# Kernel optimization log

Hardware: AMD Instinct MI355X
Metric: run time of the kernel (lower is better)

Reference implementation:

```python
import jax, jax.numpy as jnp
import numpy as np

H, BS, NB, R, K = 2048, 128, 44, 64, 8   # hidden, block_size, num_blocks, basis_rank, top_k
B, S = 4, 2048
I = NB * BS                               # intermediate size = 5632


def setup_inputs() -> dict:
    key = jax.random.key(0)
    ks = jax.random.split(key, 10)
    N = B * S
    return {
        "hidden_states": jax.random.normal(ks[0], (B, S, H), jnp.float32),
        "active_idx": jax.random.randint(ks[1], (N, K), 0, NB, jnp.int32),
        "active_score": jax.random.uniform(ks[2], (N, K), dtype=jnp.float32),
        "gate_w": jax.random.normal(ks[3], (I, H), jnp.float32) * 0.02,
        "up_w": jax.random.normal(ks[4], (I, H), jnp.float32) * 0.02,
        "down_w": jax.random.normal(ks[5], (H, I), jnp.float32) * 0.02,
        "enc_w": jax.random.normal(ks[6], (R, H), jnp.float32) * 0.02,
        "enc_b": jnp.zeros((R,), jnp.float32),
        "decoder": jax.random.normal(ks[7], (NB, R, BS), jnp.float32) * 0.02,
        "basis_bias": jnp.zeros((NB, BS), jnp.float32),
        "comp_bias": jnp.zeros((H,), jnp.float32),
        "scale": jnp.array(1.0, jnp.float32),
    }


def reference(hidden_states, active_idx, active_score, gate_w, up_w, down_w,
              enc_w, enc_b, decoder, basis_bias, comp_bias, scale):
    Bb, Ss, Hh = hidden_states.shape
    N = Bb * Ss
    x = hidden_states.reshape(N, Hh)                          # [N, H]

    # routing weights: softmax over selected block scores (all idx valid here),
    # scattered into a dense per-token per-block weight map (duplicates accumulate)
    w = jax.nn.softmax(active_score, axis=-1)                 # [N, K]
    block_w = jnp.zeros((N, NB), x.dtype).at[
        jnp.arange(N)[:, None], active_idx].add(w)            # [N, NB]

    # gated SiLU MLP intermediate over all blocks (dense equivalent of the
    # per-token block gather-compute)
    act = jax.nn.silu(x @ gate_w.T) * (x @ up_w.T)            # [N, I]

    # low-rank basis compensation: latent -> per-block block_size channels
    latent = jax.nn.silu(x @ enc_w.T + enc_b)                 # [N, R]
    comp = jnp.einsum('nr,brc->nbc', latent, decoder) + basis_bias  # [N, NB, BS]

    act_b = act.reshape(N, NB, BS) + scale * comp             # [N, NB, BS]
    weighted = (act_b * block_w[:, :, None]).reshape(N, I)    # mask+weight inactive blocks to 0

    out = weighted @ down_w.T + comp_bias                     # scatter back via down proj
    return out.reshape(Bb, Ss, Hh)
```

## Files before the change

kernel.cpp:

```cpp
#include <hip/hip_runtime.h>

#define H_  2048
#define BS_ 128
#define NB_ 44
#define R_  64
#define K_  8
#define N_  8192
#define I_  5632
#define MT  64
#define TILES 32
#define GRID_AB (8 * 6 * TILES)
#define MT2 128
#define TILES_GU 16
#define GRID_GU (8 * 6 * TILES_GU)

typedef __bf16 bf16x8 __attribute__((ext_vector_type(8)));
typedef float  f32x4  __attribute__((ext_vector_type(4)));

__device__ __forceinline__ unsigned short f2bf(float f) {
  unsigned int u = __float_as_uint(f);
  u = (u + 0x7FFFu + ((u >> 16) & 1u)) >> 16;
  return (unsigned short)u;
}
__device__ __forceinline__ float bf2f(unsigned short s) {
  return __uint_as_float(((unsigned int)s) << 16);
}
__device__ __forceinline__ bf16x8 ld8(const unsigned short* p) {
  uint4 v = *reinterpret_cast<const uint4*>(p);
  return __builtin_bit_cast(bf16x8, v);
}
__device__ __forceinline__ bf16x8 lds8(const char* p) {
  uint4 v = *reinterpret_cast<const uint4*>(p);
  return __builtin_bit_cast(bf16x8, v);
}
__device__ __forceinline__ void gl16(const void* g, void* l) {
  __builtin_amdgcn_global_load_lds(
      (const __attribute__((address_space(1))) char*)g,
      (__attribute__((address_space(3))) char*)l, 16, 0, 0);
}
#define WAIT_VM(n) do { asm volatile("s_waitcnt vmcnt(" #n ")" ::: "memory"); \
                        __builtin_amdgcn_sched_barrier(0); } while (0)
#define WAIT_LGKM0 do { asm volatile("s_waitcnt lgkmcnt(0)" ::: "memory"); \
                        __builtin_amdgcn_sched_barrier(0); } while (0)
#define SBAR __builtin_amdgcn_s_barrier()

__global__ void cvt_xgu(const float* __restrict__ x, const float* __restrict__ gw,
                        const float* __restrict__ uw, const float* __restrict__ ew,
                        const float* __restrict__ dw,
                        unsigned short* __restrict__ xb,
                        unsigned short* __restrict__ gwb,
                        unsigned short* __restrict__ uwb,
                        unsigned short* __restrict__ ewb,
                        unsigned short* __restrict__ dwb,
                        int do_down) {
  const int NX4 = N_ * H_ / 4;
  const int NG4 = I_ * H_ / 4;
  const int NE4 = R_ * H_ / 4;
  const int ND4 = H_ * I_ / 4;
  int total = NX4 + 2 * NG4 + NE4 + (do_down ? ND4 : 0);
  int stride = gridDim.x * blockDim.x;
  for (int i = blockIdx.x * blockDim.x + threadIdx.x; i < total; i += stride) {
    if (i < NX4 + 2 * NG4 + NE4) {
      const float4* s; ushort4* d; int j;
      if (i < NX4)                  { s = (const float4*)x;  d = (ushort4*)xb;  j = i; }
      else if (i < NX4 + NG4)       { s = (const float4*)gw; d = (ushort4*)gwb; j = i - NX4; }
      else if (i < NX4 + 2 * NG4)   { s = (const float4*)uw; d = (ushort4*)uwb; j = i - NX4 - NG4; }
      else                          { s = (const float4*)ew; d = (ushort4*)ewb; j = i - NX4 - 2 * NG4; }
      float4 v = s[j];
      ushort4 o; o.x = f2bf(v.x); o.y = f2bf(v.y); o.z = f2bf(v.z); o.w = f2bf(v.w);
      d[j] = o;
    } else {
      int j = i - (NX4 + 2 * NG4 + NE4);
      float4 v = ((const float4*)dw)[j];
      int flat = j * 4;
      int h = flat / I_;
      int rem = flat - h * I_;
      int b = rem >> 7, k = rem & 127;
      ushort4 o; o.x = f2bf(v.x); o.y = f2bf(v.y); o.z = f2bf(v.z); o.w = f2bf(v.w);
      *(ushort4*)(dwb + ((size_t)b * H_ + h) * BS_ + k) = o;
    }
  }
}

__global__ void cvt_down(const float* __restrict__ dw, unsigned short* __restrict__ dwb) {
  int total = H_ * I_ / 4;
  int stride = gridDim.x * blockDim.x;
  for (int i = blockIdx.x * blockDim.x + threadIdx.x; i < total; i += stride) {
    float4 v = ((const float4*)dw)[i];
    int flat = i * 4;
    int h = flat / I_;
    int rem = flat - h * I_;
    int b = rem >> 7, k = rem & 127;
    ushort4 o; o.x = f2bf(v.x); o.y = f2bf(v.y); o.z = f2bf(v.z); o.w = f2bf(v.w);
    *(ushort4*)(dwb + ((size_t)b * H_ + h) * BS_ + k) = o;
  }
}

__global__ void cvt_dec(const float* __restrict__ dec, unsigned short* __restrict__ decb) {
  int i = blockIdx.x * 256 + threadIdx.x;
  if (i >= NB_ * BS_ * R_) return;
  int b = i >> 13;
  int rem = i & 8191;
  int c = rem >> 6, r = rem & 63;
  decb[i] = f2bf(dec[(b << 13) + r * BS_ + c]);
}

__global__ void zero_counts(int* __restrict__ counts) {
  if (threadIdx.x < NB_) counts[threadIdx.x] = 0;
}

__global__ void prep_kernel(const float* __restrict__ score,
                            const int* __restrict__ aidx,
                            float* __restrict__ w_buf,
                            int* __restrict__ counts) {
  __shared__ int hist[NB_];
  int tid = threadIdx.x;
  if (tid < NB_) hist[tid] = 0;
  __syncthreads();
  int n = blockIdx.x * 256 + tid;
  float s[K_];
  float m = -1e30f;
#pragma unroll
  for (int k = 0; k < K_; k++) { s[k] = score[n * K_ + k]; m = fmaxf(m, s[k]); }
  float sum = 0.f;
#pragma unroll
  for (int k = 0; k < K_; k++) { s[k] = __expf(s[k] - m); sum += s[k]; }
  float inv = 1.f / sum;
#pragma unroll
  for (int k = 0; k < K_; k++) {
    w_buf[n * K_ + k] = s[k] * inv;
    atomicAdd(&hist[aidx[n * K_ + k]], 1);
  }
  __syncthreads();
  if (tid < NB_) atomicAdd(&counts[tid], hist[tid]);
}

__global__ void scan_kernel(const int* __restrict__ counts,
                            int* __restrict__ offsets,
                            int* __restrict__ cursors) {
  if (threadIdx.x == 0) {
    int acc = 0;
    for (int b = 0; b < NB_; b++) { offsets[b] = acc; cursors[b] = acc; acc += counts[b]; }
    offsets[NB_] = acc;
  }
}

__global__ void fill_kernel(const int* __restrict__ aidx,
                            const float* __restrict__ w_buf,
                            int* __restrict__ cursors,
                            int* __restrict__ tok_list,
                            float* __restrict__ wt_list,
                            int* __restrict__ inv) {
  int n = blockIdx.x * 256 + threadIdx.x;
#pragma unroll
  for (int k = 0; k < K_; k++) {
    int b = aidx[n * K_ + k];
    int pos = atomicAdd(&cursors[b], 1);
    tok_list[pos] = n;
    wt_list[pos] = w_buf[n * K_ + k];
    inv[n * K_ + k] = pos;
  }
}

__global__ __launch_bounds__(256) void latent_mfma(
    const unsigned short* __restrict__ xb,
    const unsigned short* __restrict__ ewb,
    const float* __restrict__ enc_b,
    unsigned short* __restrict__ lat) {
  __shared__ __align__(16) char smem[16384];
  int tid = threadIdx.x;
  int wv = tid >> 6, lane = tid & 63;
  int lo = lane & 15, hi = lane >> 4;
  int n0 = blockIdx.x * 64;

  int rowA = tid >> 2;
  int jA = (tid & 3) ^ ((rowA >> 1) & 3);
  const unsigned short* srcA = xb + (size_t)(n0 + rowA) * H_ + jA * 8;
  const unsigned short* srcB = ewb + (size_t)rowA * H_ + jA * 8;

  gl16(srcA, smem + wv * 1024);
  gl16(srcB, smem + 8192 + wv * 1024);

  f32x4 acc[4] = {};
  int cur = 0;
  for (int ks = 0; ks < H_; ks += 32) {
    if (ks + 32 < H_) {
      gl16(srcA + ks + 32, smem + (cur ^ 1) * 4096 + wv * 1024);
      gl16(srcB + ks + 32, smem + 8192 + (cur ^ 1) * 4096 + wv * 1024);
      WAIT_VM(2);
    } else {
      WAIT_VM(0);
    }
    SBAR;
    int rB = wv * 16 + lo;
    bf16x8 Bf = lds8(smem + 8192 + cur * 4096 + (rB * 4 + (hi ^ ((rB >> 1) & 3))) * 16);
#pragma unroll
    for (int m = 0; m < 4; m++) {
      int row = m * 16 + lo;
      bf16x8 Af = lds8(smem + cur * 4096 + (row * 4 + (hi ^ ((row >> 1) & 3))) * 16);
      acc[m] = __builtin_amdgcn_mfma_f32_16x16x32_bf16(Af, Bf, acc[m], 0, 0, 0);
    }
    WAIT_LGKM0;
    SBAR;
    cur ^= 1;
  }

  int r = wv * 16 + lo;
  float eb = enc_b[r];
#pragma unroll
  for (int m = 0; m < 4; m++) {
#pragma unroll
    for (int rg = 0; rg < 4; rg++) {
      int tok = n0 + m * 16 + hi * 4 + rg;
      float v = acc[m][rg] + eb;
      lat[(size_t)tok * R_ + r] = f2bf(v / (1.f + __expf(-v)));
    }
  }
}

__device__ __forceinline__ bool decode_bt(int p, int& b, int& tile) {
  b = (p & 7) + 8 * ((p >> 3) / TILES);
  tile = (p >> 3) % TILES;
  return b < NB_;
}
__device__ __forceinline__ bool decode_bt_gu(int p, int& b, int& tile) {
  b = (p & 7) + 8 * ((p >> 3) / TILES_GU);
  tile = (p >> 3) % TILES_GU;
  return b < NB_;
}

__global__ __launch_bounds__(512, 4) void gateup_kernel(
    const unsigned short* __restrict__ xb,
    const unsigned short* __restrict__ gwb,
    const unsigned short* __restrict__ uwb,
    const unsigned short* __restrict__ latb,
    const unsigned short* __restrict__ decb_all,
    const float* __restrict__ bbias,
    const float* __restrict__ scale_p,
    const int* __restrict__ counts,
    const int* __restrict__ offsets,
    const int* __restrict__ tok_list,
    const float* __restrict__ wt_list,
    unsigned short* __restrict__ actw) {
  int b, tile;
  if (!decode_bt_gu(blockIdx.x, b, tile)) return;
  int cnt = counts[b];
  int base = tile * MT2;
  if (base >= cnt) return;
  int off = offsets[b];

  __shared__ __align__(16) char smem[49152];

  int tid = threadIdx.x;
  int wv = tid >> 6, lane = tid & 63;
  int lo = lane & 15, hi = lane >> 4;
  int wr = wv >> 2, wc = wv & 3;

  int rowA = tid >> 2;
  int jA = (tid & 3) ^ ((rowA >> 1) & 3);
  int tokA = tok_list[off + min(base + rowA, cnt - 1)];
  const unsigned short* srcA = xb + (size_t)tokA * H_ + jA * 8;

  const unsigned short* gb = gwb + (size_t)b * BS_ * H_;
  const unsigned short* ub = uwb + (size_t)b * BS_ * H_;
  int cS = tid >> 2;
  int jS = (tid & 3) ^ ((cS >> 1) & 3);
  const unsigned short* srcG = gb + (size_t)cS * H_ + jS * 8;
  const unsigned short* srcU = ub + (size_t)cS * H_ + jS * 8;

  f32x4 accG[4][2] = {};
  f32x4 accU[4][2] = {};

  gl16(srcA, smem + wv * 1024);
  gl16(srcG, smem + 16384 + wv * 1024);
  gl16(srcU, smem + 32768 + wv * 1024);

  for (int it = 0; it < 64; ++it) {
    int ks = it * 32;
    if (it < 63) {
      int nb_ = (it + 1) & 1;
      gl16(srcA + ks + 32, smem + nb_ * 8192 + wv * 1024);
      gl16(srcG + ks + 32, smem + 16384 + nb_ * 8192 + wv * 1024);
      gl16(srcU + ks + 32, smem + 32768 + nb_ * 8192 + wv * 1024);
      WAIT_VM(3);
    } else {
      WAIT_VM(0);
    }
    SBAR;
    int cur = it & 1;
    bf16x8 Af[4];
#pragma unroll
    for (int m = 0; m < 4; m++) {
      int row = wr * 64 + m * 16 + lo;
      int off16 = row * 4 + (hi ^ ((row >> 1) & 3));
      Af[m] = lds8(smem + cur * 8192 + off16 * 16);
    }
    bf16x8 Gf[2], Uf[2];
#pragma unroll
    for (int cf = 0; cf < 2; cf++) {
      int c = wc * 32 + cf * 16 + lo;
      int off16 = c * 4 + (hi ^ ((c >> 1) & 3));
      Gf[cf] = lds8(smem + 16384 + cur * 8192 + off16 * 16);
      Uf[cf] = lds8(smem + 32768 + cur * 8192 + off16 * 16);
    }
#pragma unroll
    for (int m = 0; m < 4; m++) {
#pragma unroll
      for (int cf = 0; cf < 2; cf++) {
        accG[m][cf] = __builtin_amdgcn_mfma_f32_16x16x32_bf16(Af[m], Gf[cf], accG[m][cf], 0, 0, 0);
        accU[m][cf] = __builtin_amdgcn_mfma_f32_16x16x32_bf16(Af[m], Uf[cf], accU[m][cf], 0, 0, 0);
      }
    }
    WAIT_LGKM0;
    SBAR;
  }

#pragma unroll
  for (int s = 0; s < 2; s++) {
    int o = s * 512 + tid;
    int r_ = o >> 3;
    int j = (o & 7) ^ (r_ & 7);
    int tokL = tok_list[off + min(base + r_, cnt - 1)];
    gl16(latb + (size_t)tokL * R_ + j * 8, smem + 32768 + s * 8192 + wv * 1024);
  }
  const unsigned short* decb = decb_all + (size_t)b * BS_ * R_;
#pragma unroll
  for (int s = 0; s < 2; s++) {
    int o = s * 512 + tid;
    int c = o >> 3;
    int j = (o & 7) ^ (c & 7);
    gl16(decb + (size_t)c * R_ + j * 8, smem + 16384 + s * 8192 + wv * 1024);
  }
  __syncthreads();

  f32x4 accC[4][2] = {};
#pragma unroll
  for (int kk = 0; kk < 2; kk++) {
    bf16x8 L[4];
#pragma unroll
    for (int m = 0; m < 4; m++) {
      int row = wr * 64 + m * 16 + lo;
      int off16 = row * 8 + ((kk * 4 + hi) ^ (row & 7));
      L[m] = lds8(smem + 32768 + off16 * 16);
    }
#pragma unroll
    for (int cf = 0; cf < 2; cf++) {
      int c = wc * 32 + cf * 16 + lo;
      int off16 = c * 8 + ((kk * 4 + hi) ^ (c & 7));
      bf16x8 D = lds8(smem + 16384 + off16 * 16);
#pragma unroll
      for (int m = 0; m < 4; m++)
        accC[m][cf] = __builtin_amdgcn_mfma_f32_16x16x32_bf16(L[m], D, accC[m][cf], 0, 0, 0);
    }
  }

  float scal = scale_p[0];
  int cc[2] = { wc * 32 + lo, wc * 32 + 16 + lo };
  float bbv[2] = { bbias[b * BS_ + cc[0]], bbias[b * BS_ + cc[1]] };
#pragma unroll
  for (int m = 0; m < 4; m++) {
#pragma unroll
    for (int r = 0; r < 4; r++) {
      int t = wr * 64 + m * 16 + hi * 4 + r;
      int g = base + t;
      if (g < cnt) {
        float wt = wt_list[off + g];
        unsigned short* dst = actw + (size_t)(off + g) * BS_;
#pragma unroll
        for (int cf = 0; cf < 2; cf++) {
          float gg = accG[m][cf][r];
          float uu = accU[m][cf][r];
          float act = (gg / (1.f + __expf(-gg))) * uu;
          dst[cc[cf]] = f2bf((act + scal * (accC[m][cf][r] + bbv[cf])) * wt);
        }
      }
    }
  }
}

__global__ __launch_bounds__(256) void down_kernel(
    const unsigned short* __restrict__ actw,
    const unsigned short* __restrict__ dwb,
    const int* __restrict__ counts,
    const int* __restrict__ offsets,
    unsigned short* __restrict__ partial,
    int hc0, int Hc) {
  int b, tile;
  if (!decode_bt(blockIdx.x, b, tile)) return;
  int cnt = counts[b];
  int base = tile * MT;
  if (base >= cnt) return;
  int off = offsets[b];

  __shared__ __align__(16) unsigned short a_lds[MT * BS_];
  __shared__ __align__(16) char b_lds[2][16384];
  int tid = threadIdx.x;
  int wv = tid >> 6, lane = tid & 63;
  int lo = lane & 15, hi = lane >> 4;

  for (int i = tid; i < MT * BS_ / 8; i += 256) {
    int t = i >> 4, cb = i & 15;
    int g = base + t;
    uint4 v = make_uint4(0, 0, 0, 0);
    if (g < cnt) v = *(const uint4*)(actw + (size_t)(off + g) * BS_ + cb * 8);
    *(uint4*)(&a_lds[t * BS_ + ((cb ^ (t & 7)) << 3)]) = v;
  }
  __syncthreads();

  bf16x8 Bf[4][4];
#pragma unroll
  for (int kst = 0; kst < 4; kst++)
#pragma unroll
    for (int sf = 0; sf < 4; sf++) {
      int t = sf * 16 + lo, cb = kst * 4 + hi;
      Bf[kst][sf] = ld8(&a_lds[t * BS_ + ((cb ^ (t & 7)) << 3)]);
    }

  const unsigned short* db = dwb + (size_t)b * H_ * BS_;
  int rs = tid >> 4;
  int jc = tid & 15;
  {
    const unsigned short* d0 = db + (size_t)hc0 * BS_;
#pragma unroll
    for (int s = 0; s < 4; s++) {
      int r = s * 16 + rs;
      int j = jc ^ (r & 15);
      gl16(d0 + (size_t)r * BS_ + j * 8, b_lds[0] + s * 4096 + wv * 1024);
    }
  }
  __syncthreads();

  int nit = Hc >> 6;
  int cur = 0;
  for (int it = 0; it < nit; it++) {
    if (it + 1 < nit) {
      const unsigned short* dn = db + (size_t)(hc0 + (it + 1) * 64) * BS_;
#pragma unroll
      for (int s = 0; s < 4; s++) {
        int r = s * 16 + rs;
        int j = jc ^ (r & 15);
        gl16(dn + (size_t)r * BS_ + j * 8, b_lds[cur ^ 1] + s * 4096 + wv * 1024);
      }
    }
    f32x4 acc[4] = {};
    int rl = wv * 16 + lo;
#pragma unroll
    for (int kst = 0; kst < 4; kst++) {
      int cb = kst * 4 + hi;
      bf16x8 Aw = lds8(b_lds[cur] + (rl * 16 + (cb ^ lo)) * 16);
#pragma unroll
      for (int sf = 0; sf < 4; sf++)
        acc[sf] = __builtin_amdgcn_mfma_f32_16x16x32_bf16(Aw, Bf[kst][sf], acc[sf], 0, 0, 0);
    }
    int hrel = it * 64 + wv * 16 + hi * 4;
#pragma unroll
    for (int sf = 0; sf < 4; sf++) {
      int g = base + sf * 16 + lo;
      if (g < cnt) {
        uint2 pk;
        pk.x = (unsigned int)f2bf(acc[sf][0]) | ((unsigned int)f2bf(acc[sf][1]) << 16);
        pk.y = (unsigned int)f2bf(acc[sf][2]) | ((unsigned int)f2bf(acc[sf][3]) << 16);
        *(uint2*)(partial + (size_t)(off + g) * Hc + hrel) = pk;
      }
    }
    __syncthreads();
    cur ^= 1;
  }
}

__global__ __launch_bounds__(256) void reduce_kernel(
    const unsigned short* __restrict__ partial,
    const int* __restrict__ inv,
    const float* __restrict__ cbias,
    float* __restrict__ out, int hc0, int Hc) {
  int wv = threadIdx.x >> 6, l = threadIdx.x & 63;
  int n = blockIdx.x * 4 + wv;
  int rows[K_];
#pragma unroll
  for (int k = 0; k < K_; k++) rows[k] = inv[n * K_ + k];
  for (int c0w = 0; c0w < Hc; c0w += 512) {
    int cw = c0w + l * 8;
    if (cw >= Hc) continue;
    float a[8] = {0.f, 0.f, 0.f, 0.f, 0.f, 0.f, 0.f, 0.f};
#pragma unroll
    for (int k = 0; k < K_; k++) {
      uint4 v = *(const uint4*)(partial + (size_t)rows[k] * Hc + cw);
      unsigned int w0 = v.x, w1 = v.y, w2 = v.z, w3 = v.w;
      a[0] += __uint_as_float(w0 << 16); a[1] += __uint_as_float(w0 & 0xFFFF0000u);
      a[2] += __uint_as_float(w1 << 16); a[3] += __uint_as_float(w1 & 0xFFFF0000u);
      a[4] += __uint_as_float(w2 << 16); a[5] += __uint_as_float(w2 & 0xFFFF0000u);
      a[6] += __uint_as_float(w3 << 16); a[7] += __uint_as_float(w3 & 0xFFFF0000u);
    }
    int h = hc0 + cw;
    float4 c0 = *(const float4*)(cbias + h);
    float4 c1 = *(const float4*)(cbias + h + 4);
    float4 o0 = make_float4(a[0] + c0.x, a[1] + c0.y, a[2] + c0.z, a[3] + c0.w);
    float4 o1 = make_float4(a[4] + c1.x, a[5] + c1.y, a[6] + c1.z, a[7] + c1.w);
    *(float4*)(out + (size_t)n * H_ + h) = o0;
    *(float4*)(out + (size_t)n * H_ + h + 4) = o1;
  }
}

extern "C" void kernel_launch(void* const* d_in, const int* in_sizes, int n_in,
                              void* d_out, int out_size, void* d_ws, size_t ws_size,
                              hipStream_t stream) {
  const float* x       = (const float*)d_in[0];
  const int*   aidx    = (const int*)d_in[1];
  const float* score   = (const float*)d_in[2];
  const float* gate_w  = (const float*)d_in[3];
  const float* up_w    = (const float*)d_in[4];
  const float* down_w  = (const float*)d_in[5];
  const float* enc_w   = (const float*)d_in[6];
  const float* enc_b   = (const float*)d_in[7];
  const float* decoder = (const float*)d_in[8];
  const float* bbias   = (const float*)d_in[9];
  const float* cbias   = (const float*)d_in[10];
  const float* scale   = (const float*)d_in[11];
  float* out = (float*)d_out;

  char* ws = (char*)d_ws;
  const size_t OFF_GWB  = 33554432ull;
  const size_t OFF_UWB  = 56623104ull;
  const size_t OFF_DEC  = 79691776ull;
  const size_t OFF_LATB = 80412672ull;
  const size_t OFF_ENCB = 81461248ull;
  const size_t OFF_WBUF = 81723392ull;
  const size_t OFF_TOK  = 81985536ull;
  const size_t OFF_WT   = 82247680ull;
  const size_t OFF_INV  = 82509824ull;
  const size_t OFF_CNT  = 82771968ull;
  const size_t OFF_ACTW = 82772992ull;
  const size_t BASE_END = 99550208ull;
  const size_t DWB_SZ   = 23068672ull;

  unsigned short* xb   = (unsigned short*)(ws);
  unsigned short* gwb  = (unsigned short*)(ws + OFF_GWB);
  unsigned short* uwb  = (unsigned short*)(ws + OFF_UWB);
  unsigned short* decb = (unsigned short*)(ws + OFF_DEC);
  unsigned short* latb = (unsigned short*)(ws + OFF_LATB);
  unsigned short* ewb  = (unsigned short*)(ws + OFF_ENCB);
  float* w_buf         = (float*)(ws + OFF_WBUF);
  int*   tok_list      = (int*)(ws + OFF_TOK);
  float* wt_list       = (float*)(ws + OFF_WT);
  int*   inv           = (int*)(ws + OFF_INV);
  int*   counts        = (int*)(ws + OFF_CNT);
  int*   offsets       = counts + 64;
  int*   cursors       = counts + 128;
  unsigned short* actw = (unsigned short*)(ws + OFF_ACTW);

  int Hc; unsigned short* dwb; unsigned short* partial; bool early_down;
  if      (ws_size >= BASE_END + DWB_SZ + 131072ull * 512) Hc = 512;
  else if (ws_size >= BASE_END + DWB_SZ + 131072ull * 256) Hc = 256;
  else Hc = 0;
  if (Hc) {
    early_down = true;
    dwb = (unsigned short*)(ws + BASE_END);
    partial = (unsigned short*)(ws + BASE_END + DWB_SZ);
  } else {
    early_down = false;
    Hc = 256;
    dwb = gwb;
    partial = (unsigned short*)ws;
  }
  int nch = H_ / Hc;

  cvt_xgu<<<2048, 256, 0, stream>>>(x, gate_w, up_w, enc_w, down_w,
                                    xb, gwb, uwb, ewb, dwb, early_down ? 1 : 0);
  cvt_dec<<<(NB_ * BS_ * R_ + 255) / 256, 256, 0, stream>>>(decoder, decb);
  zero_counts<<<1, 64, 0, stream>>>(counts);
  prep_kernel<<<N_ / 256, 256, 0, stream>>>(score, aidx, w_buf, counts);
  scan_kernel<<<1, 64, 0, stream>>>(counts, offsets, cursors);
  fill_kernel<<<N_ / 256, 256, 0, stream>>>(aidx, w_buf, cursors, tok_list, wt_list, inv);
  latent_mfma<<<N_ / 64, 256, 0, stream>>>(xb, ewb, enc_b, latb);
  gateup_kernel<<<GRID_GU, 512, 0, stream>>>(xb, gwb, uwb, latb, decb, bbias, scale,
                                             counts, offsets, tok_list, wt_list, actw);
  if (!early_down) cvt_down<<<2048, 256, 0, stream>>>(down_w, dwb);
  for (int c = 0; c < nch; c++) {
    down_kernel<<<GRID_AB, 256, 0, stream>>>(actw, dwb, counts, offsets, partial, c * Hc, Hc);
    reduce_kernel<<<N_ / 4, 256, 0, stream>>>(partial, inv, cbias, out, c * Hc, Hc);
  }
}
```

Baseline: 548.5 us.

## Fuse down projection into gate/up kernel when workspace allows full partials

When the workspace is large enough, the gate/up kernel keeps its weighted activation tile in LDS and runs the down projection over all hidden columns directly, streaming double-buffered down_w tiles and writing bf16 partials for one reduce pass. This removes the actw round trip through global memory, the separate down_kernel launches and the chunked down/reduce loop. LDS grows to 64KB per block, which may cut occupancy. Each block now does a serial 32-step loop over the hidden dimension, which lengthens its lifetime. The fallback path now always converts down_w early instead of aliasing it onto the gate buffer.

```diff
diff --git a/kernel.cpp b/kernel.cpp
--- a/kernel.cpp
+++ b/kernel.cpp
@@ -82,20 +82,6 @@
   }
 }
 
-__global__ void cvt_down(const float* __restrict__ dw, unsigned short* __restrict__ dwb) {
-  int total = H_ * I_ / 4;
-  int stride = gridDim.x * blockDim.x;
-  for (int i = blockIdx.x * blockDim.x + threadIdx.x; i < total; i += stride) {
-    float4 v = ((const float4*)dw)[i];
-    int flat = i * 4;
-    int h = flat / I_;
-    int rem = flat - h * I_;
-    int b = rem >> 7, k = rem & 127;
-    ushort4 o; o.x = f2bf(v.x); o.y = f2bf(v.y); o.z = f2bf(v.z); o.w = f2bf(v.w);
-    *(ushort4*)(dwb + ((size_t)b * H_ + h) * BS_ + k) = o;
-  }
-}
-
 __global__ void cvt_dec(const float* __restrict__ dec, unsigned short* __restrict__ decb) {
   int i = blockIdx.x * 256 + threadIdx.x;
   if (i >= NB_ * BS_ * R_) return;
@@ -235,13 +221,16 @@
     const unsigned short* __restrict__ uwb,
     const unsigned short* __restrict__ latb,
     const unsigned short* __restrict__ decb_all,
+    const unsigned short* __restrict__ dwb,
     const float* __restrict__ bbias,
     const float* __restrict__ scale_p,
     const int* __restrict__ counts,
     const int* __restrict__ offsets,
     const int* __restrict__ tok_list,
     const float* __restrict__ wt_list,
-    unsigned short* __restrict__ actw) {
+    unsigned short* __restrict__ actw,
+    unsigned short* __restrict__ partial,
+    int fused) {
   int b, tile;
   if (!decode_bt_gu(blockIdx.x, b, tile)) return;
   int cnt = counts[b];
@@ -249,7 +238,7 @@
   if (base >= cnt) return;
   int off = offsets[b];
 
-  __shared__ __align__(16) char smem[49152];
+  __shared__ __align__(16) char smem[65536];
 
   int tid = threadIdx.x;
   int wv = tid >> 6, lane = tid & 63;
@@ -321,7 +310,7 @@
     int r_ = o >> 3;
     int j = (o & 7) ^ (r_ & 7);
     int tokL = tok_list[off + min(base + r_, cnt - 1)];
-    gl16(latb + (size_t)tokL * R_ + j * 8, smem + 32768 + s * 8192 + wv * 1024);
+    gl16(latb + (size_t)tokL * R_ + j * 8, smem + 49152 + s * 8192 + wv * 1024);
   }
   const unsigned short* decb = decb_all + (size_t)b * BS_ * R_;
 #pragma unroll
@@ -329,7 +318,7 @@
     int o = s * 512 + tid;
     int c = o >> 3;
     int j = (o & 7) ^ (c & 7);
-    gl16(decb + (size_t)c * R_ + j * 8, smem + 16384 + s * 8192 + wv * 1024);
+    gl16(decb + (size_t)c * R_ + j * 8, smem + 32768 + s * 8192 + wv * 1024);
   }
   __syncthreads();
 
@@ -341,13 +330,13 @@
     for (int m = 0; m < 4; m++) {
       int row = wr * 64 + m * 16 + lo;
       int off16 = row * 8 + ((kk * 4 + hi) ^ (row & 7));
-      L[m] = lds8(smem + 32768 + off16 * 16);
+      L[m] = lds8(smem + 49152 + off16 * 16);
     }
 #pragma unroll
     for (int cf = 0; cf < 2; cf++) {
       int c = wc * 32 + cf * 16 + lo;
       int off16 = c * 8 + ((kk * 4 + hi) ^ (c & 7));
-      bf16x8 D = lds8(smem + 16384 + off16 * 16);
+      bf16x8 D = lds8(smem + 32768 + off16 * 16);
 #pragma unroll
       for (int m = 0; m < 4; m++)
         accC[m][cf] = __builtin_amdgcn_mfma_f32_16x16x32_bf16(L[m], D, accC[m][cf], 0, 0, 0);
@@ -357,24 +346,121 @@
   float scal = scale_p[0];
   int cc[2] = { wc * 32 + lo, wc * 32 + 16 + lo };
   float bbv[2] = { bbias[b * BS_ + cc[0]], bbias[b * BS_ + cc[1]] };
+
+  if (!fused) {
+#pragma unroll
+    for (int m = 0; m < 4; m++) {
+#pragma unroll
+      for (int r = 0; r < 4; r++) {
+        int t = wr * 64 + m * 16 + hi * 4 + r;
+        int g = base + t;
+        if (g < cnt) {
+          float wt = wt_list[off + g];
+          unsigned short* dst = actw + (size_t)(off + g) * BS_;
+#pragma unroll
+          for (int cf = 0; cf < 2; cf++) {
+            float gg = accG[m][cf][r];
+            float uu = accU[m][cf][r];
+            float act = (gg / (1.f + __expf(-gg))) * uu;
+            dst[cc[cf]] = f2bf((act + scal * (accC[m][cf][r] + bbv[cf])) * wt);
+          }
+        }
+      }
+    }
+    return;
+  }
+
+  unsigned short* act_lds = (unsigned short*)smem;
 #pragma unroll
   for (int m = 0; m < 4; m++) {
 #pragma unroll
     for (int r = 0; r < 4; r++) {
       int t = wr * 64 + m * 16 + hi * 4 + r;
       int g = base + t;
+      float wt = (g < cnt) ? wt_list[off + g] : 0.f;
+#pragma unroll
+      for (int cf = 0; cf < 2; cf++) {
+        int c = cc[cf];
+        float gg = accG[m][cf][r];
+        float uu = accU[m][cf][r];
+        float act = (gg / (1.f + __expf(-gg))) * uu;
+        float a = (act + scal * (accC[m][cf][r] + bbv[cf])) * wt;
+        int cb2 = c >> 3;
+        act_lds[t * BS_ + (((cb2 ^ (t & 7)) << 3) | (c & 7))] = f2bf(a);
+      }
+    }
+  }
+  __syncthreads();
+
+  int wh = wv >> 2, ws2 = wv & 3;
+  bf16x8 Bact[4][2];
+#pragma unroll
+  for (int kst = 0; kst < 4; kst++)
+#pragma unroll
+    for (int sf = 0; sf < 2; sf++) {
+      int t = ws2 * 32 + sf * 16 + lo;
+      int cb = kst * 4 + hi;
+      Bact[kst][sf] = lds8(smem + t * 256 + ((cb ^ (t & 7)) << 4));
+    }
+
+  const unsigned short* db = dwb + (size_t)b * H_ * BS_;
+#pragma unroll
+  for (int s = 0; s < 2; s++) {
+    int o = s * 512 + tid;
+    int row = o >> 4;
+    int j = (o & 15) ^ (row & 15);
+    gl16(db + (size_t)row * BS_ + j * 8, smem + 32768 + s * 8192 + wv * 1024);
+  }
+  for (int it = 0; it < 32; ++it) {
+    int hc = it * 64;
+    if (it < 31) {
+      int nb_ = (it + 1) & 1;
+#pragma unroll
+      for (int s = 0; s < 2; s++) {
+        int o = s * 512 + tid;
+        int row = o >> 4;
+        int j = (o & 15) ^ (row & 15);
+        gl16(db + (size_t)(hc + 64 + row) * BS_ + j * 8,
+             smem + 32768 + nb_ * 16384 + s * 8192 + wv * 1024);
+      }
+      WAIT_VM(10);
+    } else {
+      WAIT_VM(8);
+    }
+    SBAR;
+    const char* bbuf = smem + 32768 + (it & 1) * 16384;
+    f32x4 acc2[2][2] = {};
+#pragma unroll
+    for (int kst = 0; kst < 4; kst++) {
+      int cb = kst * 4 + hi;
+      bf16x8 Aw[2];
+#pragma unroll
+      for (int hm = 0; hm < 2; hm++) {
+        int hr = wh * 32 + hm * 16 + lo;
+        Aw[hm] = lds8(bbuf + (hr * 16 + (cb ^ (hr & 15))) * 16);
+      }
+#pragma unroll
+      for (int hm = 0; hm < 2; hm++)
+#pragma unroll
+        for (int sf = 0; sf < 2; sf++)
+          acc2[hm][sf] = __builtin_amdgcn_mfma_f32_16x16x32_bf16(Aw[hm], Bact[kst][sf], acc2[hm][sf], 0, 0, 0);
+    }
+#pragma unroll
+    for (int sf = 0; sf < 2; sf++) {
+      int g = base + ws2 * 32 + sf * 16 + lo;
       if (g < cnt) {
-        float wt = wt_list[off + g];
-        unsigned short* dst = actw + (size_t)(off + g) * BS_;
-#pragma unroll
-        for (int cf = 0; cf < 2; cf++) {
-          float gg = accG[m][cf][r];
-          float uu = accU[m][cf][r];
-          float act = (gg / (1.f + __expf(-gg))) * uu;
-          dst[cc[cf]] = f2bf((act + scal * (accC[m][cf][r] + bbv[cf])) * wt);
+        unsigned short* pr = partial + (size_t)(off + g) * H_ + hc + wh * 32;
+#pragma unroll
+        for (int hm = 0; hm < 2; hm++) {
+          uint2 pk;
+          pk.x = (unsigned int)f2bf(acc2[hm][sf][0]) | ((unsigned int)f2bf(acc2[hm][sf][1]) << 16);
+          pk.y = (unsigned int)f2bf(acc2[hm][sf][2]) | ((unsigned int)f2bf(acc2[hm][sf][3]) << 16);
+          *(uint2*)(pr + hm * 16 + hi * 4) = pk;
         }
       }
     }
+    WAIT_LGKM0;
+    SBAR;
   }
 }
 
@@ -532,6 +618,7 @@
   const size_t OFF_ACTW = 82772992ull;
   const size_t BASE_END = 99550208ull;
   const size_t DWB_SZ   = 23068672ull;
+  const size_t PART_FULL = 268435456ull;
 
   unsigned short* xb   = (unsigned short*)(ws);
   unsigned short* gwb  = (unsigned short*)(ws + OFF_GWB);
@@ -548,35 +635,41 @@
   int*   cursors       = counts + 128;
   unsigned short* actw = (unsigned short*)(ws + OFF_ACTW);
 
+  bool fused = ws_size >= BASE_END + DWB_SZ + PART_FULL;
   int Hc; unsigned short* dwb; unsigned short* partial; bool early_down;
-  if      (ws_size >= BASE_END + DWB_SZ + 131072ull * 512) Hc = 512;
-  else if (ws_size >= BASE_END + DWB_SZ + 131072ull * 256) Hc = 256;
-  else Hc = 0;
-  if (Hc) {
+  if (fused) {
     early_down = true;
+    Hc = 2048;
+    dwb = (unsigned short*)(ws + BASE_END);
+    partial = (unsigned short*)(ws + BASE_END + DWB_SZ);
+  } else if (ws_size >= BASE_END + DWB_SZ + 131072ull * 512) {
+    early_down = true; Hc = 512;
     dwb = (unsigned short*)(ws + BASE_END);
     partial = (unsigned short*)(ws + BASE_END + DWB_SZ);
   } else {
-    early_down = false;
-    Hc = 256;
-    dwb = gwb;
+    early_down = true; Hc = 256;
+    dwb = (unsigned short*)(ws + BASE_END);
     partial = (unsigned short*)ws;
   }
-  int nch = H_ / Hc;
 
   cvt_xgu<<<2048, 256, 0, stream>>>(x, gate_w, up_w, enc_w, down_w,
-                                    xb, gwb, uwb, ewb, dwb, early_down ? 1 : 0);
+                                    xb, gwb, uwb, ewb, dwb, 1);
   cvt_dec<<<(NB_ * BS_ * R_ + 255) / 256, 256, 0, stream>>>(decoder, decb);
   zero_counts<<<1, 64, 0, stream>>>(counts);
   prep_kernel<<<N_ / 256, 256, 0, stream>>>(score, aidx, w_buf, counts);
   scan_kernel<<<1, 64, 0, stream>>>(counts, offsets, cursors);
   fill_kernel<<<N_ / 256, 256, 0, stream>>>(aidx, w_buf, cursors, tok_list, wt_list, inv);
   latent_mfma<<<N_ / 64, 256, 0, stream>>>(xb, ewb, enc_b, latb);
-  gateup_kernel<<<GRID_GU, 512, 0, stream>>>(xb, gwb, uwb, latb, decb, bbias, scale,
-                                             counts, offsets, tok_list, wt_list, actw);
-  if (!early_down) cvt_down<<<2048, 256, 0, stream>>>(down_w, dwb);
-  for (int c = 0; c < nch; c++) {
-    down_kernel<<<GRID_AB, 256, 0, stream>>>(actw, dwb, counts, offsets, partial, c * Hc, Hc);
-    reduce_kernel<<<N_ / 4, 256, 0, stream>>>(partial, inv, cbias, out, c * Hc, Hc);
-  }
-}
+  gateup_kernel<<<GRID_GU, 512, 0, stream>>>(xb, gwb, uwb, latb, decb, dwb, bbias, scale,
+                                             counts, offsets, tok_list, wt_list,
+                                             actw, partial, fused ? 1 : 0);
+  if (fused) {
+    reduce_kernel<<<N_ / 4, 256, 0, stream>>>(partial, inv, cbias, out, 0, 2048);
+  } else {
+    int nch = H_ / Hc;
+    for (int c = 0; c < nch; c++) {
+      down_kernel<<<GRID_AB, 256, 0, stream>>>(actw, dwb, counts, offsets, partial, c * Hc, Hc);
+      reduce_kernel<<<N_ / 4, 256, 0, stream>>>(partial, inv, cbias, out, c * Hc, Hc);
+    }
+  }
+}
```

Measured after the change: 604.4 us. +10.2%, slower.

## Split-K latent projection, persistent down kernel, and single-pass full-width down projection

Applied to the files above, without the earlier changes.

The latent encoder GEMM is split four ways along K, raising block count from 128 to 512, and a separate combine kernel sums the partials, adds bias and applies SiLU. The down kernel becomes a persistent grid-stride loop over 512 blocks, and when the workspace allows it runs the whole hidden width in one launch instead of several chunked launch pairs. The fallback path for the down-weight conversion is removed, so the code now always assumes the workspace can hold the converted down weights. In exchange it adds an extra fp32 partial buffer and one more launch.

```diff
diff --git a/kernel.cpp b/kernel.cpp
--- a/kernel.cpp
+++ b/kernel.cpp
@@ -9,7 +9,7 @@
 #define I_  5632
 #define MT  64
 #define TILES 32
-#define GRID_AB (8 * 6 * TILES)
+#define DOWN_GRID 512
 #define MT2 128
 #define TILES_GU 16
 #define GRID_GU (8 * 6 * TILES_GU)
@@ -51,13 +51,12 @@
                         unsigned short* __restrict__ gwb,
                         unsigned short* __restrict__ uwb,
                         unsigned short* __restrict__ ewb,
-                        unsigned short* __restrict__ dwb,
-                        int do_down) {
+                        unsigned short* __restrict__ dwb) {
   const int NX4 = N_ * H_ / 4;
   const int NG4 = I_ * H_ / 4;
   const int NE4 = R_ * H_ / 4;
   const int ND4 = H_ * I_ / 4;
-  int total = NX4 + 2 * NG4 + NE4 + (do_down ? ND4 : 0);
+  int total = NX4 + 2 * NG4 + NE4 + ND4;
   int stride = gridDim.x * blockDim.x;
   for (int i = blockIdx.x * blockDim.x + threadIdx.x; i < total; i += stride) {
     if (i < NX4 + 2 * NG4 + NE4) {
@@ -82,20 +81,6 @@
   }
 }
 
-__global__ void cvt_down(const float* __restrict__ dw, unsigned short* __restrict__ dwb) {
-  int total = H_ * I_ / 4;
-  int stride = gridDim.x * blockDim.x;
-  for (int i = blockIdx.x * blockDim.x + threadIdx.x; i < total; i += stride) {
-    float4 v = ((const float4*)dw)[i];
-    int flat = i * 4;
-    int h = flat / I_;
-    int rem = flat - h * I_;
-    int b = rem >> 7, k = rem & 127;
-    ushort4 o; o.x = f2bf(v.x); o.y = f2bf(v.y); o.z = f2bf(v.z); o.w = f2bf(v.w);
-    *(ushort4*)(dwb + ((size_t)b * H_ + h) * BS_ + k) = o;
-  }
-}
-
 __global__ void cvt_dec(const float* __restrict__ dec, unsigned short* __restrict__ decb) {
   int i = blockIdx.x * 256 + threadIdx.x;
   if (i >= NB_ * BS_ * R_) return;
@@ -165,26 +150,27 @@
 __global__ __launch_bounds__(256) void latent_mfma(
     const unsigned short* __restrict__ xb,
     const unsigned short* __restrict__ ewb,
-    const float* __restrict__ enc_b,
-    unsigned short* __restrict__ lat) {
+    float* __restrict__ lat_part) {
   __shared__ __align__(16) char smem[16384];
   int tid = threadIdx.x;
   int wv = tid >> 6, lane = tid & 63;
   int lo = lane & 15, hi = lane >> 4;
-  int n0 = blockIdx.x * 64;
+  int grp = blockIdx.x >> 2, ksl = blockIdx.x & 3;
+  int n0 = grp * 64;
+  int k0 = ksl * 512;
 
   int rowA = tid >> 2;
   int jA = (tid & 3) ^ ((rowA >> 1) & 3);
-  const unsigned short* srcA = xb + (size_t)(n0 + rowA) * H_ + jA * 8;
-  const unsigned short* srcB = ewb + (size_t)rowA * H_ + jA * 8;
+  const unsigned short* srcA = xb + (size_t)(n0 + rowA) * H_ + k0 + jA * 8;
+  const unsigned short* srcB = ewb + (size_t)rowA * H_ + k0 + jA * 8;
 
   gl16(srcA, smem + wv * 1024);
   gl16(srcB, smem + 8192 + wv * 1024);
 
   f32x4 acc[4] = {};
   int cur = 0;
-  for (int ks = 0; ks < H_; ks += 32) {
-    if (ks + 32 < H_) {
+  for (int ks = 0; ks < 512; ks += 32) {
+    if (ks + 32 < 512) {
       gl16(srcA + ks + 32, smem + (cur ^ 1) * 4096 + wv * 1024);
       gl16(srcB + ks + 32, smem + 8192 + (cur ^ 1) * 4096 + wv * 1024);
       WAIT_VM(2);
@@ -206,16 +192,25 @@
   }
 
   int r = wv * 16 + lo;
-  float eb = enc_b[r];
+  float* dst = lat_part + (size_t)ksl * N_ * R_;
 #pragma unroll
   for (int m = 0; m < 4; m++) {
 #pragma unroll
     for (int rg = 0; rg < 4; rg++) {
       int tok = n0 + m * 16 + hi * 4 + rg;
-      float v = acc[m][rg] + eb;
-      lat[(size_t)tok * R_ + r] = f2bf(v / (1.f + __expf(-v)));
-    }
-  }
+      dst[(size_t)tok * R_ + r] = acc[m][rg];
+    }
+  }
+}
+
+__global__ void latent_combine(const float* __restrict__ lp,
+                               const float* __restrict__ enc_b,
+                               unsigned short* __restrict__ lat) {
+  const int T = N_ * R_;
+  int i = blockIdx.x * 256 + threadIdx.x;
+  if (i >= T) return;
+  float v = lp[i] + lp[T + i] + lp[2 * T + i] + lp[3 * T + i] + enc_b[i & (R_ - 1)];
+  lat[i] = f2bf(v / (1.f + __expf(-v)));
 }
 
 __device__ __forceinline__ bool decode_bt(int p, int& b, int& tile) {
@@ -385,86 +380,88 @@
     const int* __restrict__ offsets,
     unsigned short* __restrict__ partial,
     int hc0, int Hc) {
-  int b, tile;
-  if (!decode_bt(blockIdx.x, b, tile)) return;
-  int cnt = counts[b];
-  int base = tile * MT;
-  if (base >= cnt) return;
-  int off = offsets[b];
-
   __shared__ __align__(16) unsigned short a_lds[MT * BS_];
   __shared__ __align__(16) char b_lds[2][16384];
   int tid = threadIdx.x;
   int wv = tid >> 6, lane = tid & 63;
   int lo = lane & 15, hi = lane >> 4;
-
-  for (int i = tid; i < MT * BS_ / 8; i += 256) {
-    int t = i >> 4, cb = i & 15;
-    int g = base + t;
-    uint4 v = make_uint4(0, 0, 0, 0);
-    if (g < cnt) v = *(const uint4*)(actw + (size_t)(off + g) * BS_ + cb * 8);
-    *(uint4*)(&a_lds[t * BS_ + ((cb ^ (t & 7)) << 3)]) = v;
-  }
-  __syncthreads();
-
-  bf16x8 Bf[4][4];
-#pragma unroll
-  for (int kst = 0; kst < 4; kst++)
-#pragma unroll
-    for (int sf = 0; sf < 4; sf++) {
-      int t = sf * 16 + lo, cb = kst * 4 + hi;
-      Bf[kst][sf] = ld8(&a_lds[t * BS_ + ((cb ^ (t & 7)) << 3)]);
-    }
-
-  const unsigned short* db = dwb + (size_t)b * H_ * BS_;
   int rs = tid >> 4;
   int jc = tid & 15;
-  {
-    const unsigned short* d0 = db + (size_t)hc0 * BS_;
-#pragma unroll
-    for (int s = 0; s < 4; s++) {
-      int r = s * 16 + rs;
-      int j = jc ^ (r & 15);
-      gl16(d0 + (size_t)r * BS_ + j * 8, b_lds[0] + s * 4096 + wv * 1024);
-    }
-  }
-  __syncthreads();
-
-  int nit = Hc >> 6;
-  int cur = 0;
-  for (int it = 0; it < nit; it++) {
-    if (it + 1 < nit) {
-      const unsigned short* dn = db + (size_t)(hc0 + (it + 1) * 64) * BS_;
+
+  for (int p = blockIdx.x; p < 8 * 6 * TILES; p += DOWN_GRID) {
+    int b, tile;
+    if (!decode_bt(p, b, tile)) continue;
+    int cnt = counts[b];
+    int base = tile * MT;
+    if (base >= cnt) continue;
+    int off = offsets[b];
+
+    for (int i = tid; i < MT * BS_ / 8; i += 256) {
+      int t = i >> 4, cb = i & 15;
+      int g = base + t;
+      uint4 v = make_uint4(0, 0, 0, 0);
+      if (g < cnt) v = *(const uint4*)(actw + (size_t)(off + g) * BS_ + cb * 8);
+      *(uint4*)(&a_lds[t * BS_ + ((cb ^ (t & 7)) << 3)]) = v;
+    }
+    __syncthreads();
+
+    bf16x8 Bf[4][4];
+#pragma unroll
+    for (int kst = 0; kst < 4; kst++)
+#pragma unroll
+      for (int sf = 0; sf < 4; sf++) {
+        int t = sf * 16 + lo, cb = kst * 4 + hi;
+        Bf[kst][sf] = ld8(&a_lds[t * BS_ + ((cb ^ (t & 7)) << 3)]);
+      }
+
+    const unsigned short* db = dwb + (size_t)b * H_ * BS_;
+    {
+      const unsigned short* d0 = db + (size_t)hc0 * BS_;
 #pragma unroll
       for (int s = 0; s < 4; s++) {
         int r = s * 16 + rs;
         int j = jc ^ (r & 15);
-        gl16(dn + (size_t)r * BS_ + j * 8, b_lds[cur ^ 1] + s * 4096 + wv * 1024);
-      }
-    }
-    f32x4 acc[4] = {};
-    int rl = wv * 16 + lo;
-#pragma unroll
-    for (int kst = 0; kst < 4; kst++) {
-      int cb = kst * 4 + hi;
-      bf16x8 Aw = lds8(b_lds[cur] + (rl * 16 + (cb ^ lo)) * 16);
-#pragma unroll
-      for (int sf = 0; sf < 4; sf++)
-        acc[sf] = __builtin_amdgcn_mfma_f32_16x16x32_bf16(Aw, Bf[kst][sf], acc[sf], 0, 0, 0);
-    }
-    int hrel = it * 64 + wv * 16 + hi * 4;
-#pragma unroll
-    for (int sf = 0; sf < 4; sf++) {
-      int g = base + sf * 16 + lo;
-      if (g < cnt) {
-        uint2 pk;
-        pk.x = (unsigned int)f2bf(acc[sf][0]) | ((unsigned int)f2bf(acc[sf][1]) << 16);
-        pk.y = (unsigned int)f2bf(acc[sf][2]) | ((unsigned int)f2bf(acc[sf][3]) << 16);
-        *(uint2*)(partial + (size_t)(off + g) * Hc + hrel) = pk;
+        gl16(d0 + (size_t)r * BS_ + j * 8, b_lds[0] + s * 4096 + wv * 1024);
       }
     }
     __syncthreads();
-    cur ^= 1;
+
+    int nit = Hc >> 6;
+    int cur = 0;
+    for (int it = 0; it < nit; it++) {
+      if (it + 1 < nit) {
+        const unsigned short* dn = db + (size_t)(hc0 + (it + 1) * 64) * BS_;
+#pragma unroll
+        for (int s = 0; s < 4; s++) {
+          int r = s * 16 + rs;
+          int j = jc ^ (r & 15);
+          gl16(dn + (size_t)r * BS_ + j * 8, b_lds[cur ^ 1] + s * 4096 + wv * 1024);
+        }
+      }
+      f32x4 acc[4] = {};
+      int rl = wv * 16 + lo;
+#pragma unroll
+      for (int kst = 0; kst < 4; kst++) {
+        int cb = kst * 4 + hi;
+        bf16x8 Aw = lds8(b_lds[cur] + (rl * 16 + (cb ^ lo)) * 16);
+#pragma unroll
+        for (int sf = 0; sf < 4; sf++)
+          acc[sf] = __builtin_amdgcn_mfma_f32_16x16x32_bf16(Aw, Bf[kst][sf], acc[sf], 0, 0, 0);
+      }
+      int hrel = it * 64 + wv * 16 + hi * 4;
+#pragma unroll
+      for (int sf = 0; sf < 4; sf++) {
+        int g = base + sf * 16 + lo;
+        if (g < cnt) {
+          uint2 pk;
+          pk.x = (unsigned int)f2bf(acc[sf][0]) | ((unsigned int)f2bf(acc[sf][1]) << 16);
+          pk.y = (unsigned int)f2bf(acc[sf][2]) | ((unsigned int)f2bf(acc[sf][3]) << 16);
+          *(uint2*)(partial + (size_t)(off + g) * Hc + hrel) = pk;
+        }
+      }
+      __syncthreads();
+      cur ^= 1;
+    }
   }
 }
 
@@ -532,6 +529,7 @@
   const size_t OFF_ACTW = 82772992ull;
   const size_t BASE_END = 99550208ull;
   const size_t DWB_SZ   = 23068672ull;
+  const size_t PART_FULL = 268435456ull;
 
   unsigned short* xb   = (unsigned short*)(ws);
   unsigned short* gwb  = (unsigned short*)(ws + OFF_GWB);
@@ -548,35 +546,30 @@
   int*   cursors       = counts + 128;
   unsigned short* actw = (unsigned short*)(ws + OFF_ACTW);
 
-  int Hc; unsigned short* dwb; unsigned short* partial; bool early_down;
-  if      (ws_size >= BASE_END + DWB_SZ + 131072ull * 512) Hc = 512;
-  else if (ws_size >= BASE_END + DWB_SZ + 131072ull * 256) Hc = 256;
-  else Hc = 0;
-  if (Hc) {
-    early_down = true;
-    dwb = (unsigned short*)(ws + BASE_END);
-    partial = (unsigned short*)(ws + BASE_END + DWB_SZ);
-  } else {
-    early_down = false;
-    Hc = 256;
-    dwb = gwb;
-    partial = (unsigned short*)ws;
-  }
-  int nch = H_ / Hc;
+  unsigned short* dwb  = (unsigned short*)(ws + BASE_END);
+  unsigned short* partial = (unsigned short*)(ws + BASE_END + DWB_SZ);
+  float* lat_part      = (float*)(ws + BASE_END + DWB_SZ);
+
+  bool full = ws_size >= BASE_END + DWB_SZ + PART_FULL;
 
   cvt_xgu<<<2048, 256, 0, stream>>>(x, gate_w, up_w, enc_w, down_w,
-                                    xb, gwb, uwb, ewb, dwb, early_down ? 1 : 0);
+                                    xb, gwb, uwb, ewb, dwb);
   cvt_dec<<<(NB_ * BS_ * R_ + 255) / 256, 256, 0, stream>>>(decoder, decb);
   zero_counts<<<1, 64, 0, stream>>>(counts);
   prep_kernel<<<N_ / 256, 256, 0, stream>>>(score, aidx, w_buf, counts);
   scan_kernel<<<1, 64, 0, stream>>>(counts, offsets, cursors);
   fill_kernel<<<N_ / 256, 256, 0, stream>>>(aidx, w_buf, cursors, tok_list, wt_list, inv);
-  latent_mfma<<<N_ / 64, 256, 0, stream>>>(xb, ewb, enc_b, latb);
+  latent_mfma<<<N_ / 16, 256, 0, stream>>>(xb, ewb, lat_part);
+  latent_combine<<<N_ * R_ / 256, 256, 0, stream>>>(lat_part, enc_b, latb);
   gateup_kernel<<<GRID_GU, 512, 0, stream>>>(xb, gwb, uwb, latb, decb, bbias, scale,
                                              counts, offsets, tok_list, wt_list, actw);
-  if (!early_down) cvt_down<<<2048, 256, 0, stream>>>(down_w, dwb);
-  for (int c = 0; c < nch; c++) {
-    down_kernel<<<GRID_AB, 256, 0, stream>>>(actw, dwb, counts, offsets, partial, c * Hc, Hc);
-    reduce_kernel<<<N_ / 4, 256, 0, stream>>>(partial, inv, cbias, out, c * Hc, Hc);
-  }
-}
+  if (full) {
+    down_kernel<<<DOWN_GRID, 256, 0, stream>>>(actw, dwb, counts, offsets, partial, 0, H_);
+    reduce_kernel<<<N_ / 4, 256, 0, stream>>>(partial, inv, cbias, out, 0, H_);
+  } else {
+    for (int c = 0; c < 4; c++) {
+      down_kernel<<<DOWN_GRID, 256, 0, stream>>>(actw, dwb, counts, offsets, partial, c * 512, 512);
+      reduce_kernel<<<N_ / 4, 256, 0, stream>>>(partial, inv, cbias, out, c * 512, 512);
+    }
+  }
+}
```

Result: no change. 546.1 us (-0.4%).
